# Performance work log

Measured on AMD Instinct MI355X. Metric: run time of the kernel, lower is better.

Reference implementation:

```python
import jax, jax.numpy as jnp
import numpy as np

N_NODES = 100000
N_EDGES = 1600000
IN_F, HID_F, OUT_F = 256, 128, 32


def spmm(rows, cols, vals, x):
    # out[i] = sum_{e: rows[e]==i} vals[e] * x[cols[e]]  -- COO SpMM
    msgs = vals[:, None] * x[cols]            # [E, F] gathered weighted messages
    return jax.ops.segment_sum(msgs, rows, num_segments=N_NODES)


def setup_inputs() -> dict:
    key = jax.random.key(0)
    k = jax.random.split(key, 6)
    x = jax.random.normal(k[0], (N_NODES, IN_F), dtype=jnp.float32)
    adj_rows = jax.random.randint(k[1], (N_EDGES,), 0, N_NODES, dtype=jnp.int32)
    adj_cols = jax.random.randint(k[2], (N_EDGES,), 0, N_NODES, dtype=jnp.int32)
    adj_vals = jax.random.uniform(k[3], (N_EDGES,), dtype=jnp.float32)
    W1 = jax.random.normal(k[4], (IN_F, HID_F), dtype=jnp.float32) / np.sqrt(IN_F)
    W2 = jax.random.normal(k[5], (HID_F, OUT_F), dtype=jnp.float32) / np.sqrt(HID_F)
    return {"x": x, "adj_rows": adj_rows, "adj_cols": adj_cols,
            "adj_vals": adj_vals, "W1": W1, "W2": W2}


def reference(x, adj_rows, adj_cols, adj_vals, W1, W2):
    # TwoLayerGCN forward (eval mode: dropout = identity, labels=None)
    h = spmm(adj_rows, adj_cols, adj_vals, x @ W1)   # conv1: linear then A_hat @
    h = jax.nn.relu(h)
    out = spmm(adj_rows, adj_cols, adj_vals, h @ W2)  # conv2
    return out
```

## Files before the change

kernel.cpp:

```cpp
#include <hip/hip_runtime.h>
#include <hip/hip_bf16.h>

#define N_NODES 100000
#define IN_F 256
#define HID_F 128
#define OUT_F 32
#define NBUCK 391
#define BCAP  5120
#define ACHUNK 4096
#define NCHUNKS ((1600000 + ACHUNK - 1) / ACHUNK)

typedef __bf16 bf16x8 __attribute__((ext_vector_type(8)));
typedef __bf16 bf16x2 __attribute__((ext_vector_type(2)));
typedef float  f32x4  __attribute__((ext_vector_type(4)));

__global__ void cvt_w1t_kernel(const float* __restrict__ W1, __bf16* __restrict__ W1T) {
    int i = blockIdx.x * 256 + threadIdx.x;
    if (i >= IN_F * HID_F) return;
    int n = i >> 8, k = i & 255;
    W1T[i] = (__bf16)W1[k * HID_F + n];
}

__device__ __forceinline__
void bucketize_body(char* smem, int blk,
                    const int* __restrict__ rows, const int* __restrict__ cols,
                    const float* __restrict__ vals, int* __restrict__ gcnt,
                    int2* __restrict__ staged, int E) {
    int2* lcv  = (int2*)smem;
    int* lcnt  = (int*)(smem + ACHUNK * 8);
    int* loff  = lcnt + NBUCK;
    int* lcur  = loff + NBUCK;
    int* gbase = lcur + NBUCK;
    int* psum  = gbase + NBUCK;

    const int t    = threadIdx.x;
    const int base = blk * ACHUNK;

    for (int b = t; b < NBUCK; b += 256) lcnt[b] = 0;
    __syncthreads();

    int myrow[16];
#pragma unroll
    for (int i = 0; i < 16; ++i) {
        int e = base + t + i * 256;
        int r = (e < E) ? rows[e] : -1;
        myrow[i] = r;
        if (r >= 0) atomicAdd(&lcnt[r >> 8], 1);
    }
    __syncthreads();

    int s0 = (t * 2     < NBUCK) ? lcnt[t * 2]     : 0;
    int s1 = (t * 2 + 1 < NBUCK) ? lcnt[t * 2 + 1] : 0;
    int local = s0 + s1;
    psum[t] = local;
    __syncthreads();
    for (int off = 1; off < 256; off <<= 1) {
        int v = (t >= off) ? psum[t - off] : 0;
        __syncthreads();
        psum[t] += v;
        __syncthreads();
    }
    int excl = psum[t] - local;
    if (t * 2     < NBUCK) { loff[t * 2]     = excl;      lcur[t * 2]     = excl; }
    if (t * 2 + 1 < NBUCK) { loff[t * 2 + 1] = excl + s0; lcur[t * 2 + 1] = excl + s0; }
    __syncthreads();

#pragma unroll
    for (int i = 0; i < 16; ++i) {
        int r = myrow[i];
        if (r >= 0) {
            int e = base + t + i * 256;
            int posl = atomicAdd(&lcur[r >> 8], 1);
            lcv[posl] = make_int2(cols[e] | ((r & 255) << 20), __float_as_int(vals[e]));
        }
    }
    __syncthreads();

    for (int b = t; b < NBUCK; b += 256) {
        int c = lcnt[b];
        gbase[b] = c ? atomicAdd(&gcnt[b], c) : 0;
    }
    __syncthreads();

    int total = loff[NBUCK - 1] + lcnt[NBUCK - 1];
    for (int i = t; i < total; i += 256) {
        int lo = 0, hi = NBUCK - 1;
        while (lo < hi) {
            int mid = (lo + hi + 1) >> 1;
            if (loff[mid] <= i) lo = mid; else hi = mid - 1;
        }
        int idx = gbase[lo] + (i - loff[lo]);
        if (idx < BCAP)
            staged[(size_t)lo * BCAP + idx] = lcv[i];
    }
}

__device__ __forceinline__
void gemm1_body(char* smem, int blk,
                const float* __restrict__ x, const __bf16* __restrict__ W1T,
                __bf16* __restrict__ xw) {
    __bf16 (*Bs)[136] = (__bf16 (*)[136])smem;
    __bf16 (*Xs)[136] = (__bf16 (*)[136])(smem + 34816);

    const int r0   = blk * 128;
    const int t    = threadIdx.x;
    const int wv   = t >> 6;
    const int lane = t & 63;
    const int quad = lane >> 4;
    const int l15  = lane & 15;

    f32x4 acc[2][8];
#pragma unroll
    for (int rt = 0; rt < 2; ++rt)
#pragma unroll
        for (int nt = 0; nt < 8; ++nt)
            acc[rt][nt] = (f32x4){0.f, 0.f, 0.f, 0.f};

    const int srow = t >> 4;
    const int soct = t & 15;

    for (int half = 0; half < 2; ++half) {
#pragma unroll
        for (int i = 0; i < 8; ++i) {
            int idx = t + i * 256;
            int n = idx >> 4, kc = idx & 15;
            bf16x8 w = *(const bf16x8*)(W1T + n * 256 + half * 128 + kc * 8);
            *(bf16x8*)(&Bs[n][kc * 8]) = w;
        }
#pragma unroll
        for (int j = 0; j < 8; ++j) {
            int row = j * 16 + srow;
            int gm = r0 + row;
            if (gm > N_NODES - 1) gm = N_NODES - 1;
            const float* xp = x + (size_t)gm * IN_F + half * 128 + soct * 8;
            float4 f0 = *(const float4*)xp;
            float4 f1 = *(const float4*)(xp + 4);
            bf16x8 v = { (__bf16)f0.x, (__bf16)f0.y, (__bf16)f0.z, (__bf16)f0.w,
                         (__bf16)f1.x, (__bf16)f1.y, (__bf16)f1.z, (__bf16)f1.w };
            *(bf16x8*)(&Xs[row][soct * 8]) = v;
        }
        __syncthreads();

#pragma unroll
        for (int kt = 0; kt < 4; ++kt) {
            const int k0 = kt * 32;
            bf16x8 a[2];
#pragma unroll
            for (int rt = 0; rt < 2; ++rt)
                a[rt] = *(const bf16x8*)(&Xs[wv * 32 + rt * 16 + l15][k0 + quad * 8]);
            bf16x8 b[8];
#pragma unroll
            for (int nt = 0; nt < 8; ++nt)
                b[nt] = *(const bf16x8*)(&Bs[nt * 16 + l15][k0 + quad * 8]);
#pragma unroll
            for (int rt = 0; rt < 2; ++rt)
#pragma unroll
                for (int nt = 0; nt < 8; ++nt)
                    acc[rt][nt] = __builtin_amdgcn_mfma_f32_16x16x32_bf16(
                        a[rt], b[nt], acc[rt][nt], 0, 0, 0);
        }
        __syncthreads();
    }

#pragma unroll
    for (int rt = 0; rt < 2; ++rt)
#pragma unroll
        for (int nt = 0; nt < 8; ++nt)
#pragma unroll
            for (int reg = 0; reg < 4; ++reg) {
                int row = r0 + wv * 32 + rt * 16 + quad * 4 + reg;
                if (row < N_NODES)
                    xw[(size_t)row * HID_F + nt * 16 + l15] = (__bf16)acc[rt][nt][reg];
            }
}

__global__ __launch_bounds__(256)
void fused_gemm1_bucketize_kernel(const float* __restrict__ x,
                                  const __bf16* __restrict__ W1T,
                                  __bf16* __restrict__ xw,
                                  const int* __restrict__ rows,
                                  const int* __restrict__ cols,
                                  const float* __restrict__ vals,
                                  int* __restrict__ gcnt,
                                  int2* __restrict__ staged, int E) {
    __shared__ __align__(16) char smem[69632];
    if (blockIdx.x < NCHUNKS)
        bucketize_body(smem, blockIdx.x, rows, cols, vals, gcnt, staged, E);
    else
        gemm1_body(smem, blockIdx.x - NCHUNKS, x, W1T, xw);
}

__global__ void scan_gcnt_kernel(const int* __restrict__ gcnt, int* __restrict__ gbase_g,
                                 int* __restrict__ row_ptr) {
    __shared__ int tmp[512];
    int t = threadIdx.x;
    int v = 0;
    if (t < NBUCK) { v = gcnt[t]; if (v > BCAP) v = BCAP; }
    tmp[t] = v;
    __syncthreads();
    for (int off = 1; off < 512; off <<= 1) {
        int u = (t >= off) ? tmp[t - off] : 0;
        __syncthreads();
        tmp[t] += u;
        __syncthreads();
    }
    if (t < NBUCK) gbase_g[t] = tmp[t] - v;
    if (t == NBUCK - 1) {
        gbase_g[NBUCK] = tmp[t];
        row_ptr[N_NODES] = tmp[t];
    }
}

__global__ __launch_bounds__(256)
void bucket_csr_kernel(const int* __restrict__ gcnt, const int* __restrict__ gbase_g,
                       const int2* __restrict__ staged,
                       int* __restrict__ row_ptr, int2* __restrict__ pedge) {
    __shared__ int2 lcv[BCAP];
    __shared__ int lcnt[256], loff[256], lcur[256];

    const int b = blockIdx.x;
    const int t = threadIdx.x;
    int n = gcnt[b]; if (n > BCAP) n = BCAP;
    const int2* sp = staged + (size_t)b * BCAP;

    lcnt[t] = 0;
    __syncthreads();
    for (int i = t; i < n; i += 256) {
        int2 v = sp[i];
        lcv[i] = v;
        atomicAdd(&lcnt[(v.x >> 20) & 255], 1);
    }
    __syncthreads();

    int v = lcnt[t];
    loff[t] = v;
    __syncthreads();
    for (int off = 1; off < 256; off <<= 1) {
        int u = (t >= off) ? loff[t - off] : 0;
        __syncthreads();
        loff[t] += u;
        __syncthreads();
    }
    int excl = loff[t] - v;
    lcur[t] = excl;
    __syncthreads();

    const int base = gbase_g[b];
    int row = (b << 8) + t;
    if (row < N_NODES) row_ptr[row] = base + excl;

    for (int i = t; i < n; i += 256) {
        int2 cv = lcv[i];
        int r = (cv.x >> 20) & 255;
        int pos = atomicAdd(&lcur[r], 1);
        pedge[base + pos] = make_int2(cv.x & 0xFFFFF, cv.y);
    }
}

__global__ __launch_bounds__(256)
void gemm2_mfma_kernel(const __bf16* __restrict__ h,
                       const float* __restrict__ W2,
                       __bf16* __restrict__ hw) {
    const int r0   = blockIdx.x * 128;
    const int wv   = threadIdx.x >> 6;
    const int lane = threadIdx.x & 63;
    const int quad = lane >> 4;
    const int l15  = lane & 15;

    __shared__ __bf16 W2T[32][136];

    for (int i = threadIdx.x; i < 32 * 128; i += 256) {
        int n = i & 31, k = i >> 5;
        W2T[n][k] = (__bf16)W2[k * OUT_F + n];
    }
    __syncthreads();

    f32x4 acc[2][2];
#pragma unroll
    for (int rt = 0; rt < 2; ++rt)
#pragma unroll
        for (int nt = 0; nt < 2; ++nt)
            acc[rt][nt] = (f32x4){0.f, 0.f, 0.f, 0.f};

#pragma unroll
    for (int kt = 0; kt < 4; ++kt) {
        const int k0 = kt * 32;
        bf16x8 a[2];
#pragma unroll
        for (int rt = 0; rt < 2; ++rt) {
            int gm = r0 + wv * 32 + rt * 16 + l15;
            if (gm > N_NODES - 1) gm = N_NODES - 1;
            a[rt] = *(const bf16x8*)(h + (size_t)gm * HID_F + k0 + quad * 8);
        }
        bf16x8 b[2];
#pragma unroll
        for (int nt = 0; nt < 2; ++nt)
            b[nt] = *(const bf16x8*)(&W2T[nt * 16 + l15][k0 + quad * 8]);
#pragma unroll
        for (int rt = 0; rt < 2; ++rt)
#pragma unroll
            for (int nt = 0; nt < 2; ++nt)
                acc[rt][nt] = __builtin_amdgcn_mfma_f32_16x16x32_bf16(
                    a[rt], b[nt], acc[rt][nt], 0, 0, 0);
    }

#pragma unroll
    for (int rt = 0; rt < 2; ++rt)
#pragma unroll
        for (int nt = 0; nt < 2; ++nt)
#pragma unroll
            for (int reg = 0; reg < 4; ++reg) {
                int row = r0 + wv * 32 + rt * 16 + quad * 4 + reg;
                if (row < N_NODES)
                    hw[(size_t)row * OUT_F + nt * 16 + l15] = (__bf16)acc[rt][nt][reg];
            }
}

__global__ __launch_bounds__(256)
void spmm1_kernel(const int* __restrict__ row_ptr,
                  const int2* __restrict__ pedge,
                  const __bf16* __restrict__ src,
                  __bf16* __restrict__ dst) {
    int row = __builtin_amdgcn_readfirstlane(blockIdx.x * 4 + (threadIdx.x >> 6));
    int lane = threadIdx.x & 63;
    if (row >= N_NODES) return;

    const int e0 = row_ptr[row];
    const int e1 = row_ptr[row + 1];

    float a0 = 0.f, a1 = 0.f;
    for (int e = e0; e < e1; e += 8) {
        int2 p[8];
#pragma unroll
        for (int j = 0; j < 8; ++j) {
            int ee = e + j;
            if (ee >= e1) ee = e1 - 1;
            p[j] = pedge[ee];
            if (e + j >= e1) p[j].y = 0;
        }
        bf16x2 s[8];
#pragma unroll
        for (int j = 0; j < 8; ++j)
            s[j] = ((const bf16x2*)(src + (size_t)p[j].x * HID_F))[lane];
#pragma unroll
        for (int j = 0; j < 8; ++j) {
            float v = __int_as_float(p[j].y);
            a0 += v * (float)s[j].x;
            a1 += v * (float)s[j].y;
        }
    }
    a0 = fmaxf(a0, 0.f);
    a1 = fmaxf(a1, 0.f);
    bf16x2 o = { (__bf16)a0, (__bf16)a1 };
    ((bf16x2*)(dst + (size_t)row * HID_F))[lane] = o;
}

__global__ __launch_bounds__(256)
void spmm2_kernel(const int* __restrict__ row_ptr,
                  const int2* __restrict__ pedge,
                  const __bf16* __restrict__ src,
                  float* __restrict__ dst) {
    long long gid = (long long)blockIdx.x * 256 + threadIdx.x;
    int row  = (int)(gid >> 4);
    int lane = (int)(gid & 15);
    if (row >= N_NODES) return;

    const int e0 = row_ptr[row];
    const int e1 = row_ptr[row + 1];

    float a0 = 0.f, a1 = 0.f;
    for (int e = e0; e < e1; e += 8) {
        int2 p[8];
#pragma unroll
        for (int j = 0; j < 8; ++j) {
            int ee = e + j;
            if (ee >= e1) ee = e1 - 1;
            p[j] = pedge[ee];
            if (e + j >= e1) p[j].y = 0;
        }
        bf16x2 s[8];
#pragma unroll
        for (int j = 0; j < 8; ++j)
            s[j] = ((const bf16x2*)(src + (size_t)p[j].x * OUT_F))[lane];
#pragma unroll
        for (int j = 0; j < 8; ++j) {
            float v = __int_as_float(p[j].y);
            a0 += v * (float)s[j].x;
            a1 += v * (float)s[j].y;
        }
    }
    ((float2*)(dst + (size_t)row * OUT_F))[lane] = make_float2(a0, a1);
}

extern "C" void kernel_launch(void* const* d_in, const int* in_sizes, int n_in,
                              void* d_out, int out_size, void* d_ws, size_t ws_size,
                              hipStream_t stream) {
    const float* x        = (const float*)d_in[0];
    const int*   adj_rows = (const int*)d_in[1];
    const int*   adj_cols = (const int*)d_in[2];
    const float* adj_vals = (const float*)d_in[3];
    const float* W1       = (const float*)d_in[4];
    const float* W2       = (const float*)d_in[5];
    float*       out      = (float*)d_out;
    const int E = in_sizes[1];

    char* p = (char*)d_ws;
    __bf16* W1T  = (__bf16*)p;  p += (size_t)IN_F * HID_F * sizeof(__bf16);
    __bf16* xw   = (__bf16*)p;  p += (size_t)N_NODES * HID_F * sizeof(__bf16);
    __bf16* h    = (__bf16*)p;  p += (size_t)N_NODES * HID_F * sizeof(__bf16);
    __bf16* hw   = (__bf16*)p;  p += (size_t)N_NODES * OUT_F * sizeof(__bf16);
    int*   row_ptr = (int*)p;   p += (size_t)(N_NODES + 1) * sizeof(int);
    int*   gcnt    = (int*)p;   p += ((NBUCK + 255) & ~255) * sizeof(int);
    int*   gbase_g = (int*)p;   p += ((NBUCK + 1 + 255) & ~255) * sizeof(int);
    p = (char*)(((uintptr_t)p + 15) & ~(uintptr_t)15);
    int2*  pedge   = (int2*)p;  p += (size_t)E * sizeof(int2);
    p = (char*)(((uintptr_t)p + 15) & ~(uintptr_t)15);
    int2*  staged  = (int2*)p;  p += (size_t)NBUCK * BCAP * sizeof(int2);

    hipMemsetAsync(gcnt, 0, (size_t)NBUCK * sizeof(int), stream);
    cvt_w1t_kernel<<<(IN_F * HID_F + 255) / 256, 256, 0, stream>>>(W1, W1T);

    fused_gemm1_bucketize_kernel<<<NCHUNKS + (N_NODES + 127) / 128, 256, 0, stream>>>(
        x, W1T, xw, adj_rows, adj_cols, adj_vals, gcnt, staged, E);

    scan_gcnt_kernel<<<1, 512, 0, stream>>>(gcnt, gbase_g, row_ptr);
    bucket_csr_kernel<<<NBUCK, 256, 0, stream>>>(gcnt, gbase_g, staged, row_ptr, pedge);

    spmm1_kernel<<<(N_NODES + 3) / 4, 256, 0, stream>>>(row_ptr, pedge, xw, h);

    gemm2_mfma_kernel<<<(N_NODES + 127) / 128, 256, 0, stream>>>(h, W2, hw);
    {
        long long threads = (long long)N_NODES * 16;
        spmm2_kernel<<<(int)((threads + 255) / 256), 256, 0, stream>>>(
            row_ptr, pedge, hw, out);
    }
}
```

Before: 313.3 us.

## Halve fused-kernel LDS, read W1 from global in GEMM1, fold bucket scan into CSR

Halves the bucketize chunk size and drops the shared-memory copy of W1T in GEMM1, so B fragments are loaded straight from global/L2. This cuts the fused kernel's LDS from about 68 KB to 34 KB to raise occupancy. The separate single-block scan kernel is removed; each bucket_csr block now recomputes the prefix over bucket counts itself, saving one launch at the cost of redundant scan work per block. The trade-offs are more global loads of W1T per MFMA step and more atomics on the global counters, since there are twice as many chunks.

```diff
diff --git a/kernel.cpp b/kernel.cpp
--- a/kernel.cpp
+++ b/kernel.cpp
@@ -7,7 +7,7 @@
 #define OUT_F 32
 #define NBUCK 391
 #define BCAP  5120
-#define ACHUNK 4096
+#define ACHUNK 2048
 #define NCHUNKS ((1600000 + ACHUNK - 1) / ACHUNK)
 
 typedef __bf16 bf16x8 __attribute__((ext_vector_type(8)));
@@ -39,9 +39,9 @@
     for (int b = t; b < NBUCK; b += 256) lcnt[b] = 0;
     __syncthreads();
 
-    int myrow[16];
-#pragma unroll
-    for (int i = 0; i < 16; ++i) {
+    int myrow[8];
+#pragma unroll
+    for (int i = 0; i < 8; ++i) {
         int e = base + t + i * 256;
         int r = (e < E) ? rows[e] : -1;
         myrow[i] = r;
@@ -66,7 +66,7 @@
     __syncthreads();
 
 #pragma unroll
-    for (int i = 0; i < 16; ++i) {
+    for (int i = 0; i < 8; ++i) {
         int r = myrow[i];
         if (r >= 0) {
             int e = base + t + i * 256;
@@ -99,8 +99,7 @@
 void gemm1_body(char* smem, int blk,
                 const float* __restrict__ x, const __bf16* __restrict__ W1T,
                 __bf16* __restrict__ xw) {
-    __bf16 (*Bs)[136] = (__bf16 (*)[136])smem;
-    __bf16 (*Xs)[136] = (__bf16 (*)[136])(smem + 34816);
+    __bf16 (*Xs)[136] = (__bf16 (*)[136])smem;
 
     const int r0   = blk * 128;
     const int t    = threadIdx.x;
@@ -120,13 +119,6 @@
     const int soct = t & 15;
 
     for (int half = 0; half < 2; ++half) {
-#pragma unroll
-        for (int i = 0; i < 8; ++i) {
-            int idx = t + i * 256;
-            int n = idx >> 4, kc = idx & 15;
-            bf16x8 w = *(const bf16x8*)(W1T + n * 256 + half * 128 + kc * 8);
-            *(bf16x8*)(&Bs[n][kc * 8]) = w;
-        }
 #pragma unroll
         for (int j = 0; j < 8; ++j) {
             int row = j * 16 + srow;
@@ -151,7 +143,8 @@
             bf16x8 b[8];
 #pragma unroll
             for (int nt = 0; nt < 8; ++nt)
-                b[nt] = *(const bf16x8*)(&Bs[nt * 16 + l15][k0 + quad * 8]);
+                b[nt] = *(const bf16x8*)(W1T + (size_t)(nt * 16 + l15) * 256
+                                              + half * 128 + k0 + quad * 8);
 #pragma unroll
             for (int rt = 0; rt < 2; ++rt)
 #pragma unroll
@@ -183,45 +176,46 @@
                                   const float* __restrict__ vals,
                                   int* __restrict__ gcnt,
                                   int2* __restrict__ staged, int E) {
-    __shared__ __align__(16) char smem[69632];
+    __shared__ __align__(16) char smem[34816];
     if (blockIdx.x < NCHUNKS)
         bucketize_body(smem, blockIdx.x, rows, cols, vals, gcnt, staged, E);
     else
         gemm1_body(smem, blockIdx.x - NCHUNKS, x, W1T, xw);
 }
 
-__global__ void scan_gcnt_kernel(const int* __restrict__ gcnt, int* __restrict__ gbase_g,
-                                 int* __restrict__ row_ptr) {
-    __shared__ int tmp[512];
-    int t = threadIdx.x;
-    int v = 0;
-    if (t < NBUCK) { v = gcnt[t]; if (v > BCAP) v = BCAP; }
-    tmp[t] = v;
-    __syncthreads();
-    for (int off = 1; off < 512; off <<= 1) {
-        int u = (t >= off) ? tmp[t - off] : 0;
-        __syncthreads();
-        tmp[t] += u;
-        __syncthreads();
-    }
-    if (t < NBUCK) gbase_g[t] = tmp[t] - v;
-    if (t == NBUCK - 1) {
-        gbase_g[NBUCK] = tmp[t];
-        row_ptr[N_NODES] = tmp[t];
-    }
-}
-
 __global__ __launch_bounds__(256)
-void bucket_csr_kernel(const int* __restrict__ gcnt, const int* __restrict__ gbase_g,
+void bucket_csr_kernel(const int* __restrict__ gcnt,
                        const int2* __restrict__ staged,
                        int* __restrict__ row_ptr, int2* __restrict__ pedge) {
     __shared__ int2 lcv[BCAP];
     __shared__ int lcnt[256], loff[256], lcur[256];
+    __shared__ int psum[256];
+    __shared__ int boff[NBUCK + 1];
 
     const int b = blockIdx.x;
     const int t = threadIdx.x;
+
+    int c0 = (t * 2     < NBUCK) ? min(gcnt[t * 2],     BCAP) : 0;
+    int c1 = (t * 2 + 1 < NBUCK) ? min(gcnt[t * 2 + 1], BCAP) : 0;
+    int local = c0 + c1;
+    psum[t] = local;
+    __syncthreads();
+    for (int off = 1; off < 256; off <<= 1) {
+        int v = (t >= off) ? psum[t - off] : 0;
+        __syncthreads();
+        psum[t] += v;
+        __syncthreads();
+    }
+    int excl = psum[t] - local;
+    if (t * 2     < NBUCK)  boff[t * 2]     = excl;
+    if (t * 2 + 1 <= NBUCK) boff[t * 2 + 1] = excl + c0;
+    __syncthreads();
+
     int n = gcnt[b]; if (n > BCAP) n = BCAP;
     const int2* sp = staged + (size_t)b * BCAP;
+    const int base = boff[b];
+
+    if (b == NBUCK - 1 && t == 0) row_ptr[N_NODES] = boff[NBUCK];
 
     lcnt[t] = 0;
     __syncthreads();
@@ -241,13 +235,12 @@
         loff[t] += u;
         __syncthreads();
     }
-    int excl = loff[t] - v;
-    lcur[t] = excl;
-    __syncthreads();
-
-    const int base = gbase_g[b];
+    int excl2 = loff[t] - v;
+    lcur[t] = excl2;
+    __syncthreads();
+
     int row = (b << 8) + t;
-    if (row < N_NODES) row_ptr[row] = base + excl;
+    if (row < N_NODES) row_ptr[row] = base + excl2;
 
     for (int i = t; i < n; i += 256) {
         int2 cv = lcv[i];
@@ -411,7 +404,6 @@
     __bf16* hw   = (__bf16*)p;  p += (size_t)N_NODES * OUT_F * sizeof(__bf16);
     int*   row_ptr = (int*)p;   p += (size_t)(N_NODES + 1) * sizeof(int);
     int*   gcnt    = (int*)p;   p += ((NBUCK + 255) & ~255) * sizeof(int);
-    int*   gbase_g = (int*)p;   p += ((NBUCK + 1 + 255) & ~255) * sizeof(int);
     p = (char*)(((uintptr_t)p + 15) & ~(uintptr_t)15);
     int2*  pedge   = (int2*)p;  p += (size_t)E * sizeof(int2);
     p = (char*)(((uintptr_t)p + 15) & ~(uintptr_t)15);
@@ -423,8 +415,7 @@
     fused_gemm1_bucketize_kernel<<<NCHUNKS + (N_NODES + 127) / 128, 256, 0, stream>>>(
         x, W1T, xw, adj_rows, adj_cols, adj_vals, gcnt, staged, E);
 
-    scan_gcnt_kernel<<<1, 512, 0, stream>>>(gcnt, gbase_g, row_ptr);
-    bucket_csr_kernel<<<NBUCK, 256, 0, stream>>>(gcnt, gbase_g, staged, row_ptr, pedge);
+    bucket_csr_kernel<<<NBUCK, 256, 0, stream>>>(gcnt, staged, row_ptr, pedge);
 
     spmm1_kernel<<<(N_NODES + 3) / 4, 256, 0, stream>>>(row_ptr, pedge, xw, h);
 
```

Result: slower. 349.2 us (+11.5%).
